# Kernel optimization log

Measured on AMD Instinct MI355X. Metric: run time of the kernel, lower is better.

## Reference

```python
import jax, jax.numpy as jnp
import numpy as np

ALPHA = 0.0001
BETA = 0.75
K_CONST = 1.0
N_WIN = 5


def setup_inputs() -> dict:
    key = jax.random.key(0)
    x = jax.random.normal(key, (64, 56, 56, 192), dtype=jnp.float32)
    return {"x": x}


def reference(x):
    # Faithful reproduction of the (buggy) keras LRN:
    #   head = max(c - half_n, 0)
    #   tail = min(c + half_n, C)
    #   window = x_sqr[..., head : c + tail + 1]  (end clipped to C by slicing)
    C = x.shape[-1]
    half_n = N_WIN // 2
    x_sqr = x * x
    # Exclusive-prefix cumsum along channels: cs[..., j] = sum of x_sqr[..., :j]
    cs = jnp.concatenate(
        [jnp.zeros(x.shape[:-1] + (1,), x.dtype), jnp.cumsum(x_sqr, axis=-1)],
        axis=-1,
    )  # [B,H,W,C+1]
    c = np.arange(C)
    head = np.maximum(c - half_n, 0)
    tail = np.minimum(c + half_n, C)
    end = np.minimum(c + tail + 1, C)  # python slicing clips the stop index
    # windowed sum-of-squares per output channel via prefix-sum difference
    scale = cs[..., end] - cs[..., head]  # [B,H,W,C]
    scale = (scale * (ALPHA / N_WIN) + K_CONST) ** BETA
    return x / scale
```

## Files before the change

### kernel.cpp

```cpp
#include <hip/hip_runtime.h>


constexpr int   C    = 192;
constexpr int   LPP  = 16;
constexpr int   CPL  = 12;
constexpr int   PPW  = 4;
constexpr int   WPB  = 4;
constexpr int   PPB  = PPW * WPB;
constexpr int   BLOCK = 256;
constexpr int   S    = 100;
constexpr float AON  = 0.0001f / 5.0f;

__global__ __launch_bounds__(BLOCK, 8) void lrn_kernel(
    const float* __restrict__ x, float* __restrict__ out, int npix) {
  __shared__ __align__(16) float oddcs[WPB * PPW * S];

  const int tid  = threadIdx.x;
  const int lane = tid & 63;
  const int w    = tid >> 6;
  const int sub  = lane & 15;
  const int pl   = lane >> 4;

  long long pix = (long long)blockIdx.x * PPB + w * PPW + pl;
  if (pix > npix - 1) pix = npix - 1;

  const float4* __restrict__ xb = (const float4*)(x + (size_t)pix * C);
  float4* __restrict__ ob       = (float4*)(out + (size_t)pix * C);

  const float4 v0 = xb[sub * 3 + 0];
  const float4 v1 = xb[sub * 3 + 1];
  const float4 v2 = xb[sub * 3 + 2];
  float xr[CPL] = {v0.x, v0.y, v0.z, v0.w, v1.x, v1.y, v1.z, v1.w,
                   v2.x, v2.y, v2.z, v2.w};

  float ta = 0.0f, tb = 0.0f;
#pragma unroll
  for (int k = 0; k < CPL; k += 2) {
    ta = fmaf(xr[k], xr[k], ta);
    tb = fmaf(xr[k + 1], xr[k + 1], tb);
  }
  const float T = ta + tb;

  float incl = T;
#pragma unroll
  for (int off = 1; off < LPP; off <<= 1) {
    const float t = __shfl_up(incl, off, LPP);
    if (sub >= off) incl += t;
  }
  const float base  = incl - T;
  const float total = __shfl(incl, LPP - 1, LPP);

  float pre[CPL];
  float run = base;
#pragma unroll
  for (int k = 0; k < CPL; ++k) {
    pre[k] = run;
    run = fmaf(xr[k], xr[k], run);
  }

  float hb0 = __shfl_up(pre[CPL - 2], 1, LPP);
  float hb1 = __shfl_up(pre[CPL - 1], 1, LPP);
  if (sub == 0) { hb0 = 0.0f; hb1 = 0.0f; }

  float* tab = &oddcs[(w * PPW + pl) * S];
  {
    float2* tp = (float2*)&tab[6 * sub];
    tp[0] = make_float2(pre[1], pre[3]);
    tp[1] = make_float2(pre[5], pre[7]);
    tp[2] = make_float2(pre[9], pre[11]);
  }
  __syncthreads();

#pragma unroll
  for (int g = 0; g < 3; ++g) {
    float q[4];
#pragma unroll
    for (int kk = 0; kk < 4; ++kk) {
      const int k = g * 4 + kk;
      const int c = CPL * sub + k;
      const float csh = (k >= 2) ? pre[k - 2] : (k == 0 ? hb0 : hb1);
      const float cse = (c < 95) ? tab[c + 1] : total;
      const float eps = (cse - csh) * AON;
      const float inv = fmaf(eps, fmaf(eps, fmaf(eps, -0.6015625f, 0.65625f), -0.75f), 1.0f);
      q[kk] = xr[k] * inv;
    }
    ob[sub * 3 + g] = make_float4(q[0], q[1], q[2], q[3]);
  }
}

extern "C" void kernel_launch(void* const* d_in, const int* in_sizes, int n_in,
                              void* d_out, int out_size, void* d_ws, size_t ws_size,
                              hipStream_t stream) {
  const float* x   = (const float*)d_in[0];
  float*       out = (float*)d_out;
  const int npix = in_sizes[0] / C;
  const int grid = (npix + PPB - 1) / PPB;
  lrn_kernel<<<grid, BLOCK, 0, stream>>>(x, out, npix);
}
```

Baseline: 260.6 us.

## Replace shared-memory table with ds_bpermute gathers and process two pixels per lane

Drops the LDS prefix table and __syncthreads, fetching neighbouring odd prefix sums from other lanes with ds_bpermute instead. Each wavefront now handles two pixels, with all six vector loads issued before any compute to raise memory-level parallelism. The occupancy hint in launch_bounds falls from 8 to 6. The cost is more registers and twelve cross-lane permutes per pixel.

```diff
diff --git a/kernel.cpp b/kernel.cpp
--- a/kernel.cpp
+++ b/kernel.cpp
@@ -1,38 +1,22 @@
 #include <hip/hip_runtime.h>
 
 
-constexpr int   C    = 192;
-constexpr int   LPP  = 16;
-constexpr int   CPL  = 12;
-constexpr int   PPW  = 4;
-constexpr int   WPB  = 4;
-constexpr int   PPB  = PPW * WPB;
+constexpr int   C     = 192;
+constexpr int   LPP   = 16;
+constexpr int   CPL   = 12;
+constexpr int   PPW   = 4;
+constexpr int   NB    = 2;
+constexpr int   WPB   = 4;
+constexpr int   PPB   = PPW * NB * WPB;
 constexpr int   BLOCK = 256;
-constexpr int   S    = 100;
-constexpr float AON  = 0.0001f / 5.0f;
+constexpr float AON   = 0.0001f / 5.0f;
 
-__global__ __launch_bounds__(BLOCK, 8) void lrn_kernel(
-    const float* __restrict__ x, float* __restrict__ out, int npix) {
-  __shared__ __align__(16) float oddcs[WPB * PPW * S];
+__device__ __forceinline__ float bperm(int byteaddr, float v) {
+  return __int_as_float(__builtin_amdgcn_ds_bpermute(byteaddr, __float_as_int(v)));
+}
 
-  const int tid  = threadIdx.x;
-  const int lane = tid & 63;
-  const int w    = tid >> 6;
-  const int sub  = lane & 15;
-  const int pl   = lane >> 4;
-
-  long long pix = (long long)blockIdx.x * PPB + w * PPW + pl;
-  if (pix > npix - 1) pix = npix - 1;
-
-  const float4* __restrict__ xb = (const float4*)(x + (size_t)pix * C);
-  float4* __restrict__ ob       = (float4*)(out + (size_t)pix * C);
-
-  const float4 v0 = xb[sub * 3 + 0];
-  const float4 v1 = xb[sub * 3 + 1];
-  const float4 v2 = xb[sub * 3 + 2];
-  float xr[CPL] = {v0.x, v0.y, v0.z, v0.w, v1.x, v1.y, v1.z, v1.w,
-                   v2.x, v2.y, v2.z, v2.w};
-
+__device__ __forceinline__ void lrn_pixel(const float xr[CPL], float4* __restrict__ ob,
+                                          int sub, int adr0, int adr1, int adr2) {
   float ta = 0.0f, tb = 0.0f;
 #pragma unroll
   for (int k = 0; k < CPL; k += 2) {
@@ -62,30 +46,75 @@
   float hb1 = __shfl_up(pre[CPL - 1], 1, LPP);
   if (sub == 0) { hb0 = 0.0f; hb1 = 0.0f; }
 
-  float* tab = &oddcs[(w * PPW + pl) * S];
-  {
-    float2* tp = (float2*)&tab[6 * sub];
-    tp[0] = make_float2(pre[1], pre[3]);
-    tp[1] = make_float2(pre[5], pre[7]);
-    tp[2] = make_float2(pre[9], pre[11]);
-  }
-  __syncthreads();
+  float g[CPL];
+  g[0]  = bperm(adr0, pre[3]);
+  g[1]  = bperm(adr0, pre[5]);
+  g[2]  = bperm(adr0, pre[7]);
+  g[3]  = bperm(adr0, pre[9]);
+  g[4]  = bperm(adr0, pre[11]);
+  g[5]  = bperm(adr1, pre[1]);
+  g[6]  = bperm(adr1, pre[3]);
+  g[7]  = bperm(adr1, pre[5]);
+  g[8]  = bperm(adr1, pre[7]);
+  g[9]  = bperm(adr1, pre[9]);
+  g[10] = bperm(adr1, pre[11]);
+  g[11] = bperm(adr2, pre[1]);
 
 #pragma unroll
-  for (int g = 0; g < 3; ++g) {
+  for (int g3 = 0; g3 < 3; ++g3) {
     float q[4];
 #pragma unroll
     for (int kk = 0; kk < 4; ++kk) {
-      const int k = g * 4 + kk;
+      const int k = g3 * 4 + kk;
       const int c = CPL * sub + k;
       const float csh = (k >= 2) ? pre[k - 2] : (k == 0 ? hb0 : hb1);
-      const float cse = (c < 95) ? tab[c + 1] : total;
+      const float cse = (c < 95) ? g[k] : total;
       const float eps = (cse - csh) * AON;
       const float inv = fmaf(eps, fmaf(eps, fmaf(eps, -0.6015625f, 0.65625f), -0.75f), 1.0f);
       q[kk] = xr[k] * inv;
     }
-    ob[sub * 3 + g] = make_float4(q[0], q[1], q[2], q[3]);
+    ob[sub * 3 + g3] = make_float4(q[0], q[1], q[2], q[3]);
   }
+}
+
+__global__ __launch_bounds__(BLOCK, 6) void lrn_kernel(
+    const float* __restrict__ x, float* __restrict__ out, int npix) {
+  const int tid  = threadIdx.x;
+  const int lane = tid & 63;
+  const int w    = tid >> 6;
+  const int sub  = lane & 15;
+  const int pl   = lane >> 4;
+
+  long long p0 = (long long)blockIdx.x * PPB + w * (PPW * NB) + pl;
+  long long p1 = p0 + PPW;
+  if (p0 > npix - 1) p0 = npix - 1;
+  if (p1 > npix - 1) p1 = npix - 1;
+
+  const float4* __restrict__ xb0 = (const float4*)(x + (size_t)p0 * C);
+  const float4* __restrict__ xb1 = (const float4*)(x + (size_t)p1 * C);
+  float4* __restrict__ ob0 = (float4*)(out + (size_t)p0 * C);
+  float4* __restrict__ ob1 = (float4*)(out + (size_t)p1 * C);
+
+  const float4 u0 = xb0[sub * 3 + 0];
+  const float4 u1 = xb0[sub * 3 + 1];
+  const float4 u2 = xb0[sub * 3 + 2];
+  const float4 v0 = xb1[sub * 3 + 0];
+  const float4 v1 = xb1[sub * 3 + 1];
+  const float4 v2 = xb1[sub * 3 + 2];
+
+  const int gb   = lane & 48;
+  const int s2   = sub * 2;
+  const int adr0 = (gb | (s2 & 15)) << 2;
+  const int adr1 = (gb | ((s2 + 1) & 15)) << 2;
+  const int adr2 = (gb | ((s2 + 2) & 15)) << 2;
+
+  float xr0[CPL] = {u0.x, u0.y, u0.z, u0.w, u1.x, u1.y, u1.z, u1.w,
+                    u2.x, u2.y, u2.z, u2.w};
+  lrn_pixel(xr0, ob0, sub, adr0, adr1, adr2);
+
+  float xr1[CPL] = {v0.x, v0.y, v0.z, v0.w, v1.x, v1.y, v1.z, v1.w,
+                    v2.x, v2.y, v2.z, v2.w};
+  lrn_pixel(xr1, ob1, sub, adr0, adr1, adr2);
 }
 
 extern "C" void kernel_launch(void* const* d_in, const int* in_sizes, int n_in,
```

New measurement: 266.8 us. 2.4% more time.
